# Performance work log

Measured on AMD Instinct MI355X. Metric: run time of the kernel, lower is better.

The kernel has to match this reference:

```python
import jax, jax.numpy as jnp
import numpy as np

NUM_NODES = 50000
IN_CH = 64
OUT_CH = 64
NUM_EDGES = 800000


def setup_inputs() -> dict:
    key = jax.random.key(0)
    k1, k2, k3, k4 = jax.random.split(key, 4)
    x = jax.random.normal(k1, (NUM_NODES, IN_CH), dtype=jnp.float32)
    edge_index = jax.random.randint(k2, (2, NUM_EDGES), 0, NUM_NODES, dtype=jnp.int64)
    # Xavier-uniform linear weight [out, 2*in], zero bias (torch convention W @ x^T + b)
    fan_in, fan_out = 2 * IN_CH, OUT_CH
    limit = np.sqrt(6.0 / (fan_in + fan_out))
    W = jax.random.uniform(k3, (OUT_CH, 2 * IN_CH), minval=-limit, maxval=limit, dtype=jnp.float32)
    b = jnp.zeros((OUT_CH,), dtype=jnp.float32)
    return {"x": x, "edge_index": edge_index, "W": W, "b": b}


def reference(x, edge_index, W, b):
    num_nodes = x.shape[0]
    row, col = edge_index[0], edge_index[1]
    # mean aggregation: scatter-add of x[row] into destination col, divide by degree
    aggr = jax.ops.segment_sum(x[row], col, num_segments=num_nodes)  # [N, C]
    deg = jax.ops.segment_sum(jnp.ones_like(col, dtype=x.dtype), col, num_segments=num_nodes)
    aggr = aggr / jnp.clip(deg, 1.0, None)[:, None]
    out = jnp.concatenate([x, aggr], axis=-1)  # [N, 2C]
    return out @ W.T + b
```

## Files before the change

kernel.cpp:

```cpp
#include <hip/hip_runtime.h>
#include <hip/hip_fp8.h>

#define NN 50000
#define NC 64
#define NE 800000
#define NGRP 3125
#define CAP 62
#define CONV_BLK 3125
#define FILL_BLK 391
#define EPB 2048
#define NPART 196
#define QCAP 4608
#define TS 288

typedef __attribute__((ext_vector_type(8))) short bf16x8;
typedef __attribute__((ext_vector_type(4))) float f32x4;

__device__ __forceinline__ unsigned short f32_to_bf16_rne(float v) {
    unsigned u = __float_as_uint(v);
    u = (u + 0x7fffu + ((u >> 16) & 1u)) >> 16;
    return (unsigned short)u;
}
__device__ __forceinline__ unsigned pack_bf16x2(float lo, float hi) {
    return (unsigned)f32_to_bf16_rne(lo) | ((unsigned)f32_to_bf16_rne(hi) << 16);
}

__device__ __forceinline__ unsigned char f32_to_fp8(float v) {
    __hip_fp8_e4m3 t(v);
    return (unsigned char)t.__x;
}
__device__ __forceinline__ float fp8_to_f32(unsigned b) {
    __hip_fp8_e4m3 t;
    t.__x = (__hip_fp8_storage_t)b;
    return (float)t;
}

__global__ __launch_bounds__(256) void convert_partition_kernel(
        const float4* __restrict__ x4, ushort4* __restrict__ xh4,
        unsigned* __restrict__ xf8,
        const int4* __restrict__ row4, const int4* __restrict__ col4,
        int* __restrict__ qcnt, unsigned* __restrict__ queue,
        const float4* __restrict__ W4, ushort4* __restrict__ wb4) {
    int b = blockIdx.x;
    if (b >= FILL_BLK + CONV_BLK) {
#pragma unroll
        for (int j = 0; j < 8; ++j) {
            int i = threadIdx.x + 256 * j;
            float4 v = W4[i];
            ushort4 h;
            h.x = f32_to_bf16_rne(v.x); h.y = f32_to_bf16_rne(v.y);
            h.z = f32_to_bf16_rne(v.z); h.w = f32_to_bf16_rne(v.w);
            wb4[i] = h;
        }
        return;
    }
    if (b >= FILL_BLK) {
        int i = (b - FILL_BLK) * 256 + threadIdx.x;
        float4 v = x4[i];
        ushort4 h;
        h.x = f32_to_bf16_rne(v.x); h.y = f32_to_bf16_rne(v.y);
        h.z = f32_to_bf16_rne(v.z); h.w = f32_to_bf16_rne(v.w);
        xh4[i] = h;
        unsigned q = (unsigned)f32_to_fp8(v.x)
                   | ((unsigned)f32_to_fp8(v.y) << 8)
                   | ((unsigned)f32_to_fp8(v.z) << 16)
                   | ((unsigned)f32_to_fp8(v.w) << 24);
        xf8[i] = q;
        return;
    }
    __shared__ int lcnt[NPART];
    __shared__ int lstart[NPART];
    __shared__ int sbase[NPART];
    __shared__ int wpart[4];
    __shared__ int stot;
    __shared__ unsigned staged[EPB];

    const int tid = threadIdx.x;
    for (int i = tid; i < NPART; i += 256) lcnt[i] = 0;
    __syncthreads();

    unsigned ent[8];
    int      rk[8];
    int      nv[2];
#pragma unroll
    for (int j = 0; j < 2; ++j) {
        int t = b * (EPB / 4) + j * 256 + tid;
        nv[j] = (t < NE / 4);
        if (nv[j]) {
            int4 r = row4[t];
            int4 c = col4[t];
            int p;
            p = c.x >> 8; ent[j*4+0] = ((unsigned)p << 24) | ((unsigned)(c.x & 255) << 16) | (unsigned)r.x;
            rk[j*4+0] = atomicAdd(&lcnt[p], 1);
            p = c.y >> 8; ent[j*4+1] = ((unsigned)p << 24) | ((unsigned)(c.y & 255) << 16) | (unsigned)r.y;
            rk[j*4+1] = atomicAdd(&lcnt[p], 1);
            p = c.z >> 8; ent[j*4+2] = ((unsigned)p << 24) | ((unsigned)(c.z & 255) << 16) | (unsigned)r.z;
            rk[j*4+2] = atomicAdd(&lcnt[p], 1);
            p = c.w >> 8; ent[j*4+3] = ((unsigned)p << 24) | ((unsigned)(c.w & 255) << 16) | (unsigned)r.w;
            rk[j*4+3] = atomicAdd(&lcnt[p], 1);
        }
    }
    __syncthreads();

    int v = (tid < NPART) ? lcnt[tid] : 0;
    int sc = v;
    const int lane2 = tid & 63;
#pragma unroll
    for (int d = 1; d < 64; d <<= 1) {
        int u = __shfl_up(sc, (unsigned)d, 64);
        if (lane2 >= d) sc += u;
    }
    if (lane2 == 63) wpart[tid >> 6] = sc;
    __syncthreads();
    {
        int wid2 = tid >> 6;
        int add = 0;
        if (wid2 > 0) add += wpart[0];
        if (wid2 > 1) add += wpart[1];
        if (wid2 > 2) add += wpart[2];
        int incl = sc + add;
        if (tid < NPART) {
            lstart[tid] = incl - v;
            sbase[tid]  = atomicAdd(&qcnt[tid], v);
        }
        if (tid == 255) stot = incl;
    }
    __syncthreads();

#pragma unroll
    for (int j = 0; j < 2; ++j) {
        if (nv[j]) {
#pragma unroll
            for (int k = 0; k < 4; ++k) {
                unsigned e = ent[j*4+k];
                staged[lstart[e >> 24] + rk[j*4+k]] = e;
            }
        }
    }
    __syncthreads();

    int tot = stot;
    for (int i = tid; i < tot; i += 256) {
        unsigned e = staged[i];
        int p = (int)(e >> 24);
        int pos = sbase[p] + (i - lstart[p]);
        if (pos < QCAP) queue[p * QCAP + pos] = e;
    }
}

__global__ __launch_bounds__(256) void build_records_kernel(
        const int* __restrict__ qcnt, const unsigned* __restrict__ queue,
        uint4* __restrict__ rec4) {
    __shared__ __align__(16) unsigned short lslot[256 * 66];
    __shared__ int lcnt[256];
    const int p = blockIdx.x;
    const int tid = threadIdx.x;
    lcnt[tid] = 0;
    __syncthreads();

    int qn = min(qcnt[p], QCAP);
    const unsigned* q = queue + p * QCAP;
    for (int i = tid; i < qn; i += 256) {
        unsigned e = q[i];
        int n = (int)((e >> 16) & 255u);
        int pos = atomicAdd(&lcnt[n], 1);
        if (pos < CAP)
            lslot[n * 66 + pos] = (unsigned short)(e & 0xffffu);
    }
    __syncthreads();

    const unsigned* ls = (const unsigned*)lslot;
    uint4* dst = rec4 + (size_t)p * 2048;
#pragma unroll
    for (int it = 0; it < 8; ++it) {
        int i = tid + 256 * it;
        int n = i >> 3, c = i & 7;
        int base = n * 33 + 4 * c - 1;
        uint4 g;
        if (c == 0) {
            g.x = (unsigned)lcnt[n];
            g.y = ls[n * 33 + 0];
            g.z = ls[n * 33 + 1];
            g.w = ls[n * 33 + 2];
        } else {
            g.x = ls[base];
            g.y = ls[base + 1];
            g.z = ls[base + 2];
            g.w = ls[base + 3];
        }
        dst[i] = g;
    }
}

__global__ __launch_bounds__(256) void gather_mfma_kernel(
        const uint4* __restrict__ xq,
        const uint2* __restrict__ xf,
        const int*   __restrict__ rec,
        const uint4* __restrict__ Wq,
        const float* __restrict__ b,
        float*       __restrict__ out) {
    __shared__ __align__(16) char tile[16 * TS];

    const int lane = threadIdx.x & 63;
    const int w    = threadIdx.x >> 6;
    const int g8   = lane >> 3;
    const int c8   = lane & 7;
    const int mg   = lane >> 4;
    const int mc   = lane & 15;

    const float bv = b[16 * w + mc];
    const unsigned short* slots = (const unsigned short*)rec;

    {
        const int gi   = blockIdx.x;
        const int base = gi * 16;
        const int n0   = base + w * 4;

        int d0 = rec[(n0 + 0) << 5], d1 = rec[(n0 + 1) << 5],
            d2 = rec[(n0 + 2) << 5], d3 = rec[(n0 + 3) << 5];
        int l0 = min(d0, CAP), l1 = min(d1, CAP), l2 = min(d2, CAP), l3 = min(d3, CAP);
        int m  = max(max(l0, l1), max(l2, l3));
        int itn = (m + 7) >> 3;
        const int k0 = ((n0 + 0) << 6) + 2, k1 = ((n0 + 1) << 6) + 2,
                  k2 = ((n0 + 2) << 6) + 2, k3 = ((n0 + 3) << 6) + 2;

        float F0[8] = {0}, F1[8] = {0}, F2[8] = {0}, F3[8] = {0};
#define ACC8F8(F, wK, u) \
        F[0] = fmaf(wK, fp8_to_f32((u.x      ) & 0xffu), F[0]); \
        F[1] = fmaf(wK, fp8_to_f32((u.x >>  8) & 0xffu), F[1]); \
        F[2] = fmaf(wK, fp8_to_f32((u.x >> 16) & 0xffu), F[2]); \
        F[3] = fmaf(wK, fp8_to_f32((u.x >> 24)        ), F[3]); \
        F[4] = fmaf(wK, fp8_to_f32((u.y      ) & 0xffu), F[4]); \
        F[5] = fmaf(wK, fp8_to_f32((u.y >>  8) & 0xffu), F[5]); \
        F[6] = fmaf(wK, fp8_to_f32((u.y >> 16) & 0xffu), F[6]); \
        F[7] = fmaf(wK, fp8_to_f32((u.y >> 24)        ), F[7]);
        for (int it = 0, e = g8; it < itn; it += 2, e += 16) {
            int eb = e + 8;
            int a0 = (int)slots[k0 + e],  a1 = (int)slots[k1 + e],
                a2 = (int)slots[k2 + e],  a3 = (int)slots[k3 + e];
            int b0 = (int)slots[k0 + eb], b1 = (int)slots[k1 + eb],
                b2 = (int)slots[k2 + eb], b3 = (int)slots[k3 + eb];
            int sa0 = (e  < l0) ? a0 : 0;  float ma0 = (e  < l0) ? 1.f : 0.f;
            int sa1 = (e  < l1) ? a1 : 0;  float ma1 = (e  < l1) ? 1.f : 0.f;
            int sa2 = (e  < l2) ? a2 : 0;  float ma2 = (e  < l2) ? 1.f : 0.f;
            int sa3 = (e  < l3) ? a3 : 0;  float ma3 = (e  < l3) ? 1.f : 0.f;
            int sb0 = (eb < l0) ? b0 : 0;  float mb0 = (eb < l0) ? 1.f : 0.f;
            int sb1 = (eb < l1) ? b1 : 0;  float mb1 = (eb < l1) ? 1.f : 0.f;
            int sb2 = (eb < l2) ? b2 : 0;  float mb2 = (eb < l2) ? 1.f : 0.f;
            int sb3 = (eb < l3) ? b3 : 0;  float mb3 = (eb < l3) ? 1.f : 0.f;
            uint2 ua0 = xf[sa0 * 8 + c8];
            uint2 ua1 = xf[sa1 * 8 + c8];
            uint2 ua2 = xf[sa2 * 8 + c8];
            uint2 ua3 = xf[sa3 * 8 + c8];
            uint2 ub0 = xf[sb0 * 8 + c8];
            uint2 ub1 = xf[sb1 * 8 + c8];
            uint2 ub2 = xf[sb2 * 8 + c8];
            uint2 ub3 = xf[sb3 * 8 + c8];
            ACC8F8(F0, ma0, ua0) ACC8F8(F0, mb0, ub0)
            ACC8F8(F1, ma1, ua1) ACC8F8(F1, mb1, ub1)
            ACC8F8(F2, ma2, ua2) ACC8F8(F2, mb2, ub2)
            ACC8F8(F3, ma3, ua3) ACC8F8(F3, mb3, ub3)
        }
#undef ACC8F8

        bf16x8 bfrag[4];
        {
            const uint4* wr = Wq + ((16 * w + mc) * 16 + mg);
#pragma unroll
            for (int ks = 0; ks < 4; ++ks)
                bfrag[ks] = *(const bf16x8*)(wr + ks * 4);
        }

#define RED8(F) \
        _Pragma("unroll") \
        for (int j = 0; j < 8; ++j) { \
            F[j] += __shfl_xor(F[j], 8, 64); \
            F[j] += __shfl_xor(F[j], 16, 64); \
            F[j] += __shfl_xor(F[j], 32, 64); \
        }
        RED8(F0) RED8(F1) RED8(F2) RED8(F3)
#undef RED8

        float inv0 = 1.0f / fmaxf((float)d0, 1.0f);
        float inv1 = 1.0f / fmaxf((float)d1, 1.0f);
        float inv2 = 1.0f / fmaxf((float)d2, 1.0f);
        float inv3 = 1.0f / fmaxf((float)d3, 1.0f);

        if (lane < 32) {
            int nk = lane >> 3, ch = lane & 7;
            uint4 sv = xq[(n0 + nk) * 8 + ch];
            *(uint4*)(tile + (w * 4 + nk) * TS + ch * 16) = sv;
        }
        if (lane < 8) {
            uint4 mv;
            mv.x = pack_bf16x2(F0[0] * inv0, F0[1] * inv0);
            mv.y = pack_bf16x2(F0[2] * inv0, F0[3] * inv0);
            mv.z = pack_bf16x2(F0[4] * inv0, F0[5] * inv0);
            mv.w = pack_bf16x2(F0[6] * inv0, F0[7] * inv0);
            *(uint4*)(tile + (w * 4 + 0) * TS + 128 + lane * 16) = mv;
            mv.x = pack_bf16x2(F1[0] * inv1, F1[1] * inv1);
            mv.y = pack_bf16x2(F1[2] * inv1, F1[3] * inv1);
            mv.z = pack_bf16x2(F1[4] * inv1, F1[5] * inv1);
            mv.w = pack_bf16x2(F1[6] * inv1, F1[7] * inv1);
            *(uint4*)(tile + (w * 4 + 1) * TS + 128 + lane * 16) = mv;
            mv.x = pack_bf16x2(F2[0] * inv2, F2[1] * inv2);
            mv.y = pack_bf16x2(F2[2] * inv2, F2[3] * inv2);
            mv.z = pack_bf16x2(F2[4] * inv2, F2[5] * inv2);
            mv.w = pack_bf16x2(F2[6] * inv2, F2[7] * inv2);
            *(uint4*)(tile + (w * 4 + 2) * TS + 128 + lane * 16) = mv;
            mv.x = pack_bf16x2(F3[0] * inv3, F3[1] * inv3);
            mv.y = pack_bf16x2(F3[2] * inv3, F3[3] * inv3);
            mv.z = pack_bf16x2(F3[4] * inv3, F3[5] * inv3);
            mv.w = pack_bf16x2(F3[6] * inv3, F3[7] * inv3);
            *(uint4*)(tile + (w * 4 + 3) * TS + 128 + lane * 16) = mv;
        }
        __syncthreads();

        f32x4 acc = {bv, bv, bv, bv};
#pragma unroll
        for (int ks = 0; ks < 4; ++ks) {
            bf16x8 af = *(const bf16x8*)(tile + mc * TS + ks * 64 + mg * 16);
            acc = __builtin_amdgcn_mfma_f32_16x16x32_bf16(af, bfrag[ks], acc, 0, 0, 0);
        }

#pragma unroll
        for (int r = 0; r < 4; ++r)
            out[(base + mg * 4 + r) * NC + 16 * w + mc] = acc[r];
    }
}

extern "C" void kernel_launch(void* const* d_in, const int* in_sizes, int n_in,
                              void* d_out, int out_size, void* d_ws, size_t ws_size,
                              hipStream_t stream) {
    const float* x   = (const float*)d_in[0];
    const int*   ei  = (const int*)d_in[1];
    const float* W   = (const float*)d_in[2];
    const float* b   = (const float*)d_in[3];
    float*       out = (float*)d_out;

    const int* row = ei;
    const int* col = ei + NE;

    int*      qcnt  = (int*)d_ws;
    unsigned* queue = (unsigned*)(qcnt + 256);
    int*      rec   = (int*)(queue + (size_t)NPART * QCAP);
    unsigned short* xh = (unsigned short*)(rec + (size_t)50176 * 32);
    unsigned* xf8 = (unsigned*)(xh + (size_t)NN * NC);
    unsigned short* wb = (unsigned short*)(xf8 + (size_t)NN * NC / 4);

    hipMemsetAsync(qcnt, 0, 256 * sizeof(int), stream);

    convert_partition_kernel<<<FILL_BLK + CONV_BLK + 1, 256, 0, stream>>>(
        (const float4*)x, (ushort4*)xh, xf8, (const int4*)row, (const int4*)col,
        qcnt, queue, (const float4*)W, (ushort4*)wb);

    build_records_kernel<<<NPART, 256, 0, stream>>>(
        qcnt, queue, (uint4*)rec);

    gather_mfma_kernel<<<NGRP, 256, 0, stream>>>(
        (const uint4*)xh, (const uint2*)xf8, rec, (const uint4*)wb, b, out);
}
```

Before: 115.9 us.

## Use packed fp8 conversion and packed FMA, retune partition and record block sizes

The gather kernel now decodes fp8 pairs with the hardware packed-convert builtin and accumulates with v_pk_fma_f32 on float2 vectors, roughly halving the ALU instructions spent on the fp8 decode and FMA inner loop. It also gains a launch-bounds occupancy hint and loads the bias later to shorten its live range. Separately, partition blocks now handle 1024 edges each with twice as many blocks, and build_records runs 512 threads per block. The inline asm and the occupancy cap may constrain register allocation.

```diff
diff --git a/kernel.cpp b/kernel.cpp
--- a/kernel.cpp
+++ b/kernel.cpp
@@ -7,14 +7,15 @@
 #define NGRP 3125
 #define CAP 62
 #define CONV_BLK 3125
-#define FILL_BLK 391
-#define EPB 2048
+#define FILL_BLK 782
+#define EPB 1024
 #define NPART 196
 #define QCAP 4608
 #define TS 288
 
 typedef __attribute__((ext_vector_type(8))) short bf16x8;
 typedef __attribute__((ext_vector_type(4))) float f32x4;
+typedef __attribute__((ext_vector_type(2))) float f32x2;
 
 __device__ __forceinline__ unsigned short f32_to_bf16_rne(float v) {
     unsigned u = __float_as_uint(v);
@@ -33,6 +34,26 @@
     __hip_fp8_e4m3 t;
     t.__x = (__hip_fp8_storage_t)b;
     return (float)t;
+}
+
+#if __has_builtin(__builtin_amdgcn_cvt_pk_f32_fp8)
+template <bool HI>
+__device__ __forceinline__ f32x2 cvtpk(unsigned u) {
+    return __builtin_amdgcn_cvt_pk_f32_fp8(u, HI);
+}
+#else
+template <bool HI>
+__device__ __forceinline__ f32x2 cvtpk(unsigned u) {
+    f32x2 r;
+    r.x = fp8_to_f32((u >> (HI ? 16 : 0)) & 0xffu);
+    r.y = fp8_to_f32((u >> (HI ? 24 : 8)) & 0xffu);
+    return r;
+}
+#endif
+__device__ __forceinline__ f32x2 pk_fma(f32x2 a, f32x2 b, f32x2 c) {
+    f32x2 d;
+    asm("v_pk_fma_f32 %0, %1, %2, %3" : "=v"(d) : "v"(a), "v"(b), "v"(c));
+    return d;
 }
 
 __global__ __launch_bounds__(256) void convert_partition_kernel(
@@ -79,26 +100,22 @@
     for (int i = tid; i < NPART; i += 256) lcnt[i] = 0;
     __syncthreads();
 
-    unsigned ent[8];
-    int      rk[8];
-    int      nv[2];
-#pragma unroll
-    for (int j = 0; j < 2; ++j) {
-        int t = b * (EPB / 4) + j * 256 + tid;
-        nv[j] = (t < NE / 4);
-        if (nv[j]) {
-            int4 r = row4[t];
-            int4 c = col4[t];
-            int p;
-            p = c.x >> 8; ent[j*4+0] = ((unsigned)p << 24) | ((unsigned)(c.x & 255) << 16) | (unsigned)r.x;
-            rk[j*4+0] = atomicAdd(&lcnt[p], 1);
-            p = c.y >> 8; ent[j*4+1] = ((unsigned)p << 24) | ((unsigned)(c.y & 255) << 16) | (unsigned)r.y;
-            rk[j*4+1] = atomicAdd(&lcnt[p], 1);
-            p = c.z >> 8; ent[j*4+2] = ((unsigned)p << 24) | ((unsigned)(c.z & 255) << 16) | (unsigned)r.z;
-            rk[j*4+2] = atomicAdd(&lcnt[p], 1);
-            p = c.w >> 8; ent[j*4+3] = ((unsigned)p << 24) | ((unsigned)(c.w & 255) << 16) | (unsigned)r.w;
-            rk[j*4+3] = atomicAdd(&lcnt[p], 1);
-        }
+    unsigned ent[4];
+    int      rk[4];
+    int t = b * 256 + tid;
+    const int nv = (t < NE / 4);
+    if (nv) {
+        int4 r = row4[t];
+        int4 c = col4[t];
+        int p;
+        p = c.x >> 8; ent[0] = ((unsigned)p << 24) | ((unsigned)(c.x & 255) << 16) | (unsigned)r.x;
+        rk[0] = atomicAdd(&lcnt[p], 1);
+        p = c.y >> 8; ent[1] = ((unsigned)p << 24) | ((unsigned)(c.y & 255) << 16) | (unsigned)r.y;
+        rk[1] = atomicAdd(&lcnt[p], 1);
+        p = c.z >> 8; ent[2] = ((unsigned)p << 24) | ((unsigned)(c.z & 255) << 16) | (unsigned)r.z;
+        rk[2] = atomicAdd(&lcnt[p], 1);
+        p = c.w >> 8; ent[3] = ((unsigned)p << 24) | ((unsigned)(c.w & 255) << 16) | (unsigned)r.w;
+        rk[3] = atomicAdd(&lcnt[p], 1);
     }
     __syncthreads();
 
@@ -127,14 +144,11 @@
     }
     __syncthreads();
 
-#pragma unroll
-    for (int j = 0; j < 2; ++j) {
-        if (nv[j]) {
-#pragma unroll
-            for (int k = 0; k < 4; ++k) {
-                unsigned e = ent[j*4+k];
-                staged[lstart[e >> 24] + rk[j*4+k]] = e;
-            }
+    if (nv) {
+#pragma unroll
+        for (int k = 0; k < 4; ++k) {
+            unsigned e = ent[k];
+            staged[lstart[e >> 24] + rk[k]] = e;
         }
     }
     __syncthreads();
@@ -148,19 +162,19 @@
     }
 }
 
-__global__ __launch_bounds__(256) void build_records_kernel(
+__global__ __launch_bounds__(512) void build_records_kernel(
         const int* __restrict__ qcnt, const unsigned* __restrict__ queue,
         uint4* __restrict__ rec4) {
     __shared__ __align__(16) unsigned short lslot[256 * 66];
     __shared__ int lcnt[256];
     const int p = blockIdx.x;
     const int tid = threadIdx.x;
-    lcnt[tid] = 0;
+    if (tid < 256) lcnt[tid] = 0;
     __syncthreads();
 
     int qn = min(qcnt[p], QCAP);
     const unsigned* q = queue + p * QCAP;
-    for (int i = tid; i < qn; i += 256) {
+    for (int i = tid; i < qn; i += 512) {
         unsigned e = q[i];
         int n = (int)((e >> 16) & 255u);
         int pos = atomicAdd(&lcnt[n], 1);
@@ -172,8 +186,8 @@
     const unsigned* ls = (const unsigned*)lslot;
     uint4* dst = rec4 + (size_t)p * 2048;
 #pragma unroll
-    for (int it = 0; it < 8; ++it) {
-        int i = tid + 256 * it;
+    for (int it = 0; it < 4; ++it) {
+        int i = tid + 512 * it;
         int n = i >> 3, c = i & 7;
         int base = n * 33 + 4 * c - 1;
         uint4 g;
@@ -192,7 +206,7 @@
     }
 }
 
-__global__ __launch_bounds__(256) void gather_mfma_kernel(
+__global__ __launch_bounds__(256, 4) void gather_mfma_kernel(
         const uint4* __restrict__ xq,
         const uint2* __restrict__ xf,
         const int*   __restrict__ rec,
@@ -208,7 +222,6 @@
     const int mg   = lane >> 4;
     const int mc   = lane & 15;
 
-    const float bv = b[16 * w + mc];
     const unsigned short* slots = (const unsigned short*)rec;
 
     {
@@ -224,16 +237,17 @@
         const int k0 = ((n0 + 0) << 6) + 2, k1 = ((n0 + 1) << 6) + 2,
                   k2 = ((n0 + 2) << 6) + 2, k3 = ((n0 + 3) << 6) + 2;
 
-        float F0[8] = {0}, F1[8] = {0}, F2[8] = {0}, F3[8] = {0};
-#define ACC8F8(F, wK, u) \
-        F[0] = fmaf(wK, fp8_to_f32((u.x      ) & 0xffu), F[0]); \
-        F[1] = fmaf(wK, fp8_to_f32((u.x >>  8) & 0xffu), F[1]); \
-        F[2] = fmaf(wK, fp8_to_f32((u.x >> 16) & 0xffu), F[2]); \
-        F[3] = fmaf(wK, fp8_to_f32((u.x >> 24)        ), F[3]); \
-        F[4] = fmaf(wK, fp8_to_f32((u.y      ) & 0xffu), F[4]); \
-        F[5] = fmaf(wK, fp8_to_f32((u.y >>  8) & 0xffu), F[5]); \
-        F[6] = fmaf(wK, fp8_to_f32((u.y >> 16) & 0xffu), F[6]); \
-        F[7] = fmaf(wK, fp8_to_f32((u.y >> 24)        ), F[7]);
+        f32x2 G0[4], G1[4], G2[4], G3[4];
+#pragma unroll
+        for (int j = 0; j < 4; ++j) {
+            G0[j] = (f32x2)0.f; G1[j] = (f32x2)0.f;
+            G2[j] = (f32x2)0.f; G3[j] = (f32x2)0.f;
+        }
+#define ACC8F8(G, wk, u) { \
+        f32x2 p0 = cvtpk<false>(u.x), p1 = cvtpk<true>(u.x); \
+        f32x2 p2 = cvtpk<false>(u.y), p3 = cvtpk<true>(u.y); \
+        G[0] = pk_fma(wk, p0, G[0]); G[1] = pk_fma(wk, p1, G[1]); \
+        G[2] = pk_fma(wk, p2, G[2]); G[3] = pk_fma(wk, p3, G[3]); }
         for (int it = 0, e = g8; it < itn; it += 2, e += 16) {
             int eb = e + 8;
             int a0 = (int)slots[k0 + e],  a1 = (int)slots[k1 + e],
@@ -256,10 +270,18 @@
             uint2 ub1 = xf[sb1 * 8 + c8];
             uint2 ub2 = xf[sb2 * 8 + c8];
             uint2 ub3 = xf[sb3 * 8 + c8];
-            ACC8F8(F0, ma0, ua0) ACC8F8(F0, mb0, ub0)
-            ACC8F8(F1, ma1, ua1) ACC8F8(F1, mb1, ub1)
-            ACC8F8(F2, ma2, ua2) ACC8F8(F2, mb2, ub2)
-            ACC8F8(F3, ma3, ua3) ACC8F8(F3, mb3, ub3)
+            f32x2 wa0; wa0.x = ma0; wa0.y = ma0;
+            f32x2 wa1; wa1.x = ma1; wa1.y = ma1;
+            f32x2 wa2; wa2.x = ma2; wa2.y = ma2;
+            f32x2 wa3; wa3.x = ma3; wa3.y = ma3;
+            f32x2 wb0; wb0.x = mb0; wb0.y = mb0;
+            f32x2 wb1; wb1.x = mb1; wb1.y = mb1;
+            f32x2 wb2; wb2.x = mb2; wb2.y = mb2;
+            f32x2 wb3; wb3.x = mb3; wb3.y = mb3;
+            ACC8F8(G0, wa0, ua0) ACC8F8(G0, wb0, ub0)
+            ACC8F8(G1, wa1, ua1) ACC8F8(G1, wb1, ub1)
+            ACC8F8(G2, wa2, ua2) ACC8F8(G2, wb2, ub2)
+            ACC8F8(G3, wa3, ua3) ACC8F8(G3, wb3, ub3)
         }
 #undef ACC8F8
 
@@ -270,15 +292,19 @@
             for (int ks = 0; ks < 4; ++ks)
                 bfrag[ks] = *(const bf16x8*)(wr + ks * 4);
         }
-
-#define RED8(F) \
+        const float bv = b[16 * w + mc];
+
+#define RED8(G) \
         _Pragma("unroll") \
-        for (int j = 0; j < 8; ++j) { \
-            F[j] += __shfl_xor(F[j], 8, 64); \
-            F[j] += __shfl_xor(F[j], 16, 64); \
-            F[j] += __shfl_xor(F[j], 32, 64); \
-        }
-        RED8(F0) RED8(F1) RED8(F2) RED8(F3)
+        for (int j = 0; j < 4; ++j) { \
+            G[j].x += __shfl_xor(G[j].x, 8, 64); \
+            G[j].x += __shfl_xor(G[j].x, 16, 64); \
+            G[j].x += __shfl_xor(G[j].x, 32, 64); \
+            G[j].y += __shfl_xor(G[j].y, 8, 64); \
+            G[j].y += __shfl_xor(G[j].y, 16, 64); \
+            G[j].y += __shfl_xor(G[j].y, 32, 64); \
+        }
+        RED8(G0) RED8(G1) RED8(G2) RED8(G3)
 #undef RED8
 
         float inv0 = 1.0f / fmaxf((float)d0, 1.0f);
@@ -293,25 +319,25 @@
         }
         if (lane < 8) {
             uint4 mv;
-            mv.x = pack_bf16x2(F0[0] * inv0, F0[1] * inv0);
-            mv.y = pack_bf16x2(F0[2] * inv0, F0[3] * inv0);
-            mv.z = pack_bf16x2(F0[4] * inv0, F0[5] * inv0);
-            mv.w = pack_bf16x2(F0[6] * inv0, F0[7] * inv0);
+            mv.x = pack_bf16x2(G0[0].x * inv0, G0[0].y * inv0);
+            mv.y = pack_bf16x2(G0[1].x * inv0, G0[1].y * inv0);
+            mv.z = pack_bf16x2(G0[2].x * inv0, G0[2].y * inv0);
+            mv.w = pack_bf16x2(G0[3].x * inv0, G0[3].y * inv0);
             *(uint4*)(tile + (w * 4 + 0) * TS + 128 + lane * 16) = mv;
-            mv.x = pack_bf16x2(F1[0] * inv1, F1[1] * inv1);
-            mv.y = pack_bf16x2(F1[2] * inv1, F1[3] * inv1);
-            mv.z = pack_bf16x2(F1[4] * inv1, F1[5] * inv1);
-            mv.w = pack_bf16x2(F1[6] * inv1, F1[7] * inv1);
+            mv.x = pack_bf16x2(G1[0].x * inv1, G1[0].y * inv1);
+            mv.y = pack_bf16x2(G1[1].x * inv1, G1[1].y * inv1);
+            mv.z = pack_bf16x2(G1[2].x * inv1, G1[2].y * inv1);
+            mv.w = pack_bf16x2(G1[3].x * inv1, G1[3].y * inv1);
             *(uint4*)(tile + (w * 4 + 1) * TS + 128 + lane * 16) = mv;
-            mv.x = pack_bf16x2(F2[0] * inv2, F2[1] * inv2);
-            mv.y = pack_bf16x2(F2[2] * inv2, F2[3] * inv2);
-            mv.z = pack_bf16x2(F2[4] * inv2, F2[5] * inv2);
-            mv.w = pack_bf16x2(F2[6] * inv2, F2[7] * inv2);
+            mv.x = pack_bf16x2(G2[0].x * inv2, G2[0].y * inv2);
+            mv.y = pack_bf16x2(G2[1].x * inv2, G2[1].y * inv2);
+            mv.z = pack_bf16x2(G2[2].x * inv2, G2[2].y * inv2);
+            mv.w = pack_bf16x2(G2[3].x * inv2, G2[3].y * inv2);
             *(uint4*)(tile + (w * 4 + 2) * TS + 128 + lane * 16) = mv;
-            mv.x = pack_bf16x2(F3[0] * inv3, F3[1] * inv3);
-            mv.y = pack_bf16x2(F3[2] * inv3, F3[3] * inv3);
-            mv.z = pack_bf16x2(F3[4] * inv3, F3[5] * inv3);
-            mv.w = pack_bf16x2(F3[6] * inv3, F3[7] * inv3);
+            mv.x = pack_bf16x2(G3[0].x * inv3, G3[0].y * inv3);
+            mv.y = pack_bf16x2(G3[1].x * inv3, G3[1].y * inv3);
+            mv.z = pack_bf16x2(G3[2].x * inv3, G3[2].y * inv3);
+            mv.w = pack_bf16x2(G3[3].x * inv3, G3[3].y * inv3);
             *(uint4*)(tile + (w * 4 + 3) * TS + 128 + lane * 16) = mv;
         }
         __syncthreads();
@@ -348,13 +374,13 @@
     unsigned* xf8 = (unsigned*)(xh + (size_t)NN * NC);
     unsigned short* wb = (unsigned short*)(xf8 + (size_t)NN * NC / 4);
 
-    hipMemsetAsync(qcnt, 0, 256 * sizeof(int), stream);
+    (void)hipMemsetAsync(qcnt, 0, 256 * sizeof(int), stream);
 
     convert_partition_kernel<<<FILL_BLK + CONV_BLK + 1, 256, 0, stream>>>(
         (const float4*)x, (ushort4*)xh, xf8, (const int4*)row, (const int4*)col,
         qcnt, queue, (const float4*)W, (ushort4*)wb);
 
-    build_records_kernel<<<NPART, 256, 0, stream>>>(
+    build_records_kernel<<<NPART, 512, 0, stream>>>(
         qcnt, queue, (uint4*)rec);
 
     gather_mfma_kernel<<<NGRP, 256, 0, stream>>>(
```

Measured after the change: 119.2 us. 2.8% more time.
